# Kernel tuning notes

Measured on AMD Instinct MI355X. Metric: run time of the kernel, lower is better.

Reference implementation:

```python
import jax, jax.numpy as jnp
import numpy as np

B, C, H, W, K = 64, 64, 32, 32, 1024  # C == dim_dict, K == size_dict
BETA = 0.25


def setup_inputs() -> dict:
    key = jax.random.key(0)
    k1, k2, k3 = jax.random.split(key, 3)
    return {
        "z_from_encoder": jax.random.normal(k1, (B, C, H, W), dtype=jnp.float32),
        "codebook": jax.random.normal(k2, (K, C), dtype=jnp.float32),
        "codebook_weight": jax.random.normal(k3, (K,), dtype=jnp.float32),
        "flg_train": 1,
    }


def reference(z_from_encoder, codebook, codebook_weight, flg_train):
    # NCHW -> NHWC, flatten to (N, D)
    z = jnp.transpose(z_from_encoder, (0, 2, 3, 1))
    zf = z.reshape(-1, z.shape[-1])                      # (N, D)
    # squared euclidean distances via expansion (N, K)
    d = (jnp.sum(zf ** 2, axis=1, keepdims=True)
         + jnp.sum(codebook ** 2, axis=1)
         - 2.0 * zf @ codebook.T)
    idx = jnp.argmin(d, axis=1)                          # (N,)
    # one-hot @ codebook == gather
    z_q = codebook[idx].reshape(z.shape)                 # (B, H, W, D)
    if flg_train:
        loss = (BETA * jnp.mean((jax.lax.stop_gradient(z_q) - z) ** 2)
                + jnp.mean((z_q - jax.lax.stop_gradient(z)) ** 2))
    else:
        loss = jnp.float32(0.0)
    # straight-through estimator
    z_q_st = z + jax.lax.stop_gradient(z_q - z)
    # codebook usage histogram -> perplexity
    n_tok = zf.shape[0]
    e_mean = jnp.zeros((codebook.shape[0],), z.dtype).at[idx].add(1.0) / n_tok
    perplexity = jnp.exp(-jnp.sum(e_mean * jnp.log(e_mean + 1e-10)))
    z_q_out = jnp.transpose(z_q_st, (0, 3, 1, 2))        # back to NCHW
    return z_q_out, loss, perplexity
```

## Files before the change

### kernel.cpp

```cpp
#include <hip/hip_runtime.h>


typedef __attribute__((ext_vector_type(8))) short short8;
typedef __attribute__((ext_vector_type(4))) float float4v;

#define NELEM 4194304

#define WS_CBF   0
#define WS_C2H   262144
#define WS_HIST  266240
#define WS_LOSS  270336

__device__ __forceinline__ unsigned bf16_rne(float x) {
    unsigned u = __float_as_uint(x);
    return (u + 0x7fffu + ((u >> 16) & 1u)) >> 16;
}

__global__ __launch_bounds__(256) void prep_kernel(
    const float* __restrict__ cb, ushort* __restrict__ cbf,
    float* __restrict__ c2h, int* __restrict__ hist, float* __restrict__ loss_part) {
    __shared__ float s_c2[2][16];
    int tid  = threadIdx.x;
    int lane = tid & 63, wave = tid >> 6;
    int quad = lane >> 4, col = lane & 15;
    int bx   = blockIdx.x;

    if (bx >= 64) {
        hist[(bx - 64) * 256 + tid] = 0;
        if (bx == 64 && tid < 64) loss_part[tid] = 0.f;
        return;
    }
    int c = bx, fid = wave;
    int st = fid & 1, split = fid >> 1;
    int code  = c * 16 + col;
    int dbase = st * 32 + quad * 8;
    const float* cp = cb + code * 64 + dbase;
    float4v v0 = *(const float4v*)cp;
    float4v v1 = *(const float4v*)(cp + 4);
    float xs[8] = {v0.x, v0.y, v0.z, v0.w, v1.x, v1.y, v1.z, v1.w};
    short8 frag;
    float ssq = 0.f;
#pragma unroll
    for (int j = 0; j < 8; j++) {
        float x = xs[j];
        ssq = fmaf(x, x, ssq);
        unsigned hb = bf16_rne(x);
        if (split == 0) frag[j] = (short)hb;
        else            frag[j] = (short)bf16_rne(x - __uint_as_float(hb << 16));
    }
    *(short8*)(cbf + ((c * 4 + fid) * 64 + lane) * 8) = frag;
    if (split == 0) {
        ssq += __shfl_xor(ssq, 16);
        ssq += __shfl_xor(ssq, 32);
        if (quad == 0) s_c2[st][col] = ssq;
    }
    __syncthreads();
    if (tid < 16) c2h[c * 16 + tid] = -0.5f * (s_c2[0][tid] + s_c2[1][tid]);
}

__global__ __launch_bounds__(256, 4) void vq_kernel(
    const float* __restrict__ z, const float* __restrict__ cb,
    const ushort* __restrict__ cbf, const float* __restrict__ c2h,
    float* __restrict__ out, float* __restrict__ loss_part, int* __restrict__ hist)
{
    __shared__ float s_q[64 * 65];
    __shared__ float s_ms[2][64];
    __shared__ int   s_mi[2][64];
    __shared__ int   s_idx[64];
    __shared__ float s_red[4];

    int tid  = threadIdx.x;
    int lane = tid & 63, wave = tid >> 6;
    int quad = lane >> 4, col = lane & 15;
    int bx   = blockIdx.x;

    int tokbase = bx * 64;
    int bb = tokbase >> 10, hwb = tokbase & 1023;
    const float* zb = z + bb * 65536 + hwb;
    int tokhalf = wave & 1, khalf = wave >> 1;

    short8 ah[2][2], al[2][2];
#pragma unroll
    for (int g = 0; g < 2; g++) {
        int rel = tokhalf * 32 + g * 16 + col;
#pragma unroll
        for (int st = 0; st < 2; st++) {
            short8 h8, l8;
#pragma unroll
            for (int j = 0; j < 8; j++) {
                int d = st * 32 + quad * 8 + j;
                float x = zb[d * 1024 + rel];
                unsigned hb = bf16_rne(x);
                h8[j] = (short)hb;
                l8[j] = (short)bf16_rne(x - __uint_as_float(hb << 16));
            }
            ah[g][st] = h8; al[g][st] = l8;
        }
    }

    float best[2][4]; int bidx[2][4];
#pragma unroll
    for (int g = 0; g < 2; g++)
#pragma unroll
        for (int r = 0; r < 4; r++) { best[g][r] = -1e38f; bidx[g][r] = 0; }

    int cbase = khalf * 32;
    const ushort* cw = cbf + lane * 8;
    {
        const ushort* p0 = cw + cbase * 2048;
        short8 nb0 = *(const short8*)(p0 + 0);
        short8 nb1 = *(const short8*)(p0 + 512);
        short8 nb2 = *(const short8*)(p0 + 1024);
        short8 nb3 = *(const short8*)(p0 + 1536);
        float  nini = c2h[cbase * 16 + col];
        for (int cc = 0; cc < 32; cc++) {
            short8 bh0 = nb0, bh1 = nb1, bl0 = nb2, bl1 = nb3;
            float  ini = nini;
            if (cc < 31) {
                const ushort* np = cw + (cbase + cc + 1) * 2048;
                nb0 = *(const short8*)(np + 0);
                nb1 = *(const short8*)(np + 512);
                nb2 = *(const short8*)(np + 1024);
                nb3 = *(const short8*)(np + 1536);
                nini = c2h[(cbase + cc + 1) * 16 + col];
            }
            int code = (cbase + cc) * 16 + col;
#pragma unroll
            for (int g = 0; g < 2; g++) {
                float4v a0 = {ini, ini, ini, ini};
                float4v a1 = {0.f, 0.f, 0.f, 0.f};
                a0 = __builtin_amdgcn_mfma_f32_16x16x32_bf16(ah[g][0], bh0, a0, 0, 0, 0);
                a1 = __builtin_amdgcn_mfma_f32_16x16x32_bf16(ah[g][1], bh1, a1, 0, 0, 0);
                a0 = __builtin_amdgcn_mfma_f32_16x16x32_bf16(ah[g][0], bl0, a0, 0, 0, 0);
                a1 = __builtin_amdgcn_mfma_f32_16x16x32_bf16(ah[g][1], bl1, a1, 0, 0, 0);
                a0 = __builtin_amdgcn_mfma_f32_16x16x32_bf16(al[g][0], bh0, a0, 0, 0, 0);
                a1 = __builtin_amdgcn_mfma_f32_16x16x32_bf16(al[g][1], bh1, a1, 0, 0, 0);
                a0 = __builtin_amdgcn_mfma_f32_16x16x32_bf16(al[g][0], bl0, a0, 0, 0, 0);
                a1 = __builtin_amdgcn_mfma_f32_16x16x32_bf16(al[g][1], bl1, a1, 0, 0, 0);
#pragma unroll
                for (int r = 0; r < 4; r++) {
                    float s = a0[r] + a1[r];
                    if (s > best[g][r]) { best[g][r] = s; bidx[g][r] = code; }
                }
            }
        }
    }

#pragma unroll
    for (int g = 0; g < 2; g++) {
#pragma unroll
        for (int r = 0; r < 4; r++) {
            float s = best[g][r]; int ix = bidx[g][r];
#pragma unroll
            for (int m = 1; m <= 8; m <<= 1) {
                float so = __shfl_xor(s, m);
                int   io = __shfl_xor(ix, m);
                if (so > s || (so == s && io < ix)) { s = so; ix = io; }
            }
            if (col == 0) {
                int t = tokhalf * 32 + g * 16 + quad * 4 + r;
                s_ms[khalf][t] = s; s_mi[khalf][t] = ix;
            }
        }
    }
    __syncthreads();

    if (tid < 64) {
        float s0 = s_ms[0][tid], s1 = s_ms[1][tid];
        int   i0 = s_mi[0][tid], i1 = s_mi[1][tid];
        int   ix = (s1 > s0) ? i1 : i0;
        s_idx[tid] = ix;
        atomicAdd(&hist[ix], 1);
    }
    __syncthreads();

#pragma unroll
    for (int p = 0; p < 16; p++) {
        int i = p * 256 + tid;
        int t = i >> 6, d = i & 63;
        s_q[t * 65 + d] = cb[s_idx[t] * 64 + d];
    }
    __syncthreads();

    float ls = 0.f;
#pragma unroll 4
    for (int p = 0; p < 16; p++) {
        int i = p * 256 + tid;
        int d = i >> 6, t = i & 63;
        int a = d * 1024 + t;
        float zv = zb[a];
        float q  = s_q[t * 65 + d];
        float df = q - zv;
        out[bb * 65536 + hwb + a] = zv + df;
        ls = fmaf(df, df, ls);
    }
#pragma unroll
    for (int off = 32; off; off >>= 1) ls += __shfl_down(ls, off);
    if (lane == 0) s_red[wave] = ls;
    __syncthreads();
    if (tid == 0) {
        float v = (s_red[0] + s_red[1]) + (s_red[2] + s_red[3]);
        atomicAdd(&loss_part[bx & 63], v);
    }
}

__global__ __launch_bounds__(1024) void finalize_kernel(
    const int* __restrict__ hist, const float* __restrict__ loss_part,
    const int* __restrict__ flg, float* __restrict__ out) {
    __shared__ float red[16];
    int   k = threadIdx.x;
    float e = (float)hist[k] * (1.0f / 65536.0f);
    float v = e * logf(e + 1e-10f);
#pragma unroll
    for (int off = 32; off; off >>= 1) v += __shfl_down(v, off);
    if ((k & 63) == 0) red[k >> 6] = v;
    __syncthreads();
    if (k == 0) {
        float s = 0.f;
#pragma unroll
        for (int i = 0; i < 16; i++) s += red[i];
        out[NELEM + 1] = expf(-s);

        float ls = 0.f;
        for (int i = 0; i < 64; i++) ls += loss_part[i];
        float m    = ls * (1.0f / (float)NELEM);
        out[NELEM] = (*flg) ? (0.25f * m + m) : 0.0f;
    }
}

extern "C" void kernel_launch(void* const* d_in, const int* in_sizes, int n_in,
                              void* d_out, int out_size, void* d_ws, size_t ws_size,
                              hipStream_t stream) {
    const float* z   = (const float*)d_in[0];
    const float* cb  = (const float*)d_in[1];
    const int*   flg = (const int*)d_in[3];

    float* out = (float*)d_out;
    char*  ws  = (char*)d_ws;

    ushort* cbf       = (ushort*)(ws + WS_CBF);
    float*  c2h       = (float*)(ws + WS_C2H);
    int*    hist      = (int*)(ws + WS_HIST);
    float*  loss_part = (float*)(ws + WS_LOSS);

    prep_kernel<<<68, 256, 0, stream>>>(cb, cbf, c2h, hist, loss_part);
    vq_kernel<<<1024, 256, 0, stream>>>(z, cb, cbf, c2h, out, loss_part, hist);
    finalize_kernel<<<1, 1024, 0, stream>>>(hist, loss_part, flg, out);
}
```

Baseline: 121.2 us.

## Double tokens per block and fold finalize into last-block reduction

Each vq block now handles 128 tokens instead of 64, so every codebook fragment loaded from global memory feeds twice as many MFMAs. The grid drops to 512 blocks and the launch bound drops to 2 waves per SIMD to make room for the larger register and LDS footprint. The separate finalize kernel is removed: a global done-counter lets the last block compute perplexity and loss, saving one kernel launch. In exchange occupancy falls, there are fewer blocks than before to spread over the CUs, and the tail now includes a serial reduction in one block.

```diff
diff --git a/kernel.cpp b/kernel.cpp
--- a/kernel.cpp
+++ b/kernel.cpp
@@ -5,11 +5,13 @@
 typedef __attribute__((ext_vector_type(4))) float float4v;
 
 #define NELEM 4194304
+#define NBLK  512
 
 #define WS_CBF   0
 #define WS_C2H   262144
 #define WS_HIST  266240
 #define WS_LOSS  270336
+#define WS_DONE  270464
 
 __device__ __forceinline__ unsigned bf16_rne(float x) {
     unsigned u = __float_as_uint(x);
@@ -18,7 +20,8 @@
 
 __global__ __launch_bounds__(256) void prep_kernel(
     const float* __restrict__ cb, ushort* __restrict__ cbf,
-    float* __restrict__ c2h, int* __restrict__ hist, float* __restrict__ loss_part) {
+    float* __restrict__ c2h, int* __restrict__ hist, float* __restrict__ loss_part,
+    int* __restrict__ done) {
     __shared__ float s_c2[2][16];
     int tid  = threadIdx.x;
     int lane = tid & 63, wave = tid >> 6;
@@ -27,7 +30,10 @@
 
     if (bx >= 64) {
         hist[(bx - 64) * 256 + tid] = 0;
-        if (bx == 64 && tid < 64) loss_part[tid] = 0.f;
+        if (bx == 64) {
+            if (tid < 32)  loss_part[tid] = 0.f;
+            if (tid == 32) *done = 0;
+        }
         return;
     }
     int c = bx, fid = wave;
@@ -58,31 +64,33 @@
     if (tid < 16) c2h[c * 16 + tid] = -0.5f * (s_c2[0][tid] + s_c2[1][tid]);
 }
 
-__global__ __launch_bounds__(256, 4) void vq_kernel(
+__global__ __launch_bounds__(256, 2) void vq_kernel(
     const float* __restrict__ z, const float* __restrict__ cb,
     const ushort* __restrict__ cbf, const float* __restrict__ c2h,
-    float* __restrict__ out, float* __restrict__ loss_part, int* __restrict__ hist)
+    float* __restrict__ out, float* __restrict__ loss_part, int* __restrict__ hist,
+    int* __restrict__ done, const int* __restrict__ flg)
 {
-    __shared__ float s_q[64 * 65];
-    __shared__ float s_ms[2][64];
-    __shared__ int   s_mi[2][64];
-    __shared__ int   s_idx[64];
+    __shared__ float s_q[128 * 65];
+    __shared__ float s_ms[2][128];
+    __shared__ int   s_mi[2][128];
+    __shared__ int   s_idx[128];
     __shared__ float s_red[4];
+    __shared__ int   s_last;
 
     int tid  = threadIdx.x;
     int lane = tid & 63, wave = tid >> 6;
     int quad = lane >> 4, col = lane & 15;
     int bx   = blockIdx.x;
 
-    int tokbase = bx * 64;
+    int tokbase = bx * 128;
     int bb = tokbase >> 10, hwb = tokbase & 1023;
     const float* zb = z + bb * 65536 + hwb;
-    int tokhalf = wave & 1, khalf = wave >> 1;
-
-    short8 ah[2][2], al[2][2];
-#pragma unroll
-    for (int g = 0; g < 2; g++) {
-        int rel = tokhalf * 32 + g * 16 + col;
+    int tokgrp = wave & 1, khalf = wave >> 1;
+
+    short8 ah[4][2], al[4][2];
+#pragma unroll
+    for (int g = 0; g < 4; g++) {
+        int rel = tokgrp * 64 + g * 16 + col;
 #pragma unroll
         for (int st = 0; st < 2; st++) {
             short8 h8, l8;
@@ -98,9 +106,9 @@
         }
     }
 
-    float best[2][4]; int bidx[2][4];
-#pragma unroll
-    for (int g = 0; g < 2; g++)
+    float best[4][4]; int bidx[4][4];
+#pragma unroll
+    for (int g = 0; g < 4; g++)
 #pragma unroll
         for (int r = 0; r < 4; r++) { best[g][r] = -1e38f; bidx[g][r] = 0; }
 
@@ -126,7 +134,7 @@
             }
             int code = (cbase + cc) * 16 + col;
 #pragma unroll
-            for (int g = 0; g < 2; g++) {
+            for (int g = 0; g < 4; g++) {
                 float4v a0 = {ini, ini, ini, ini};
                 float4v a1 = {0.f, 0.f, 0.f, 0.f};
                 a0 = __builtin_amdgcn_mfma_f32_16x16x32_bf16(ah[g][0], bh0, a0, 0, 0, 0);
@@ -147,7 +155,7 @@
     }
 
 #pragma unroll
-    for (int g = 0; g < 2; g++) {
+    for (int g = 0; g < 4; g++) {
 #pragma unroll
         for (int r = 0; r < 4; r++) {
             float s = best[g][r]; int ix = bidx[g][r];
@@ -158,14 +166,14 @@
                 if (so > s || (so == s && io < ix)) { s = so; ix = io; }
             }
             if (col == 0) {
-                int t = tokhalf * 32 + g * 16 + quad * 4 + r;
+                int t = tokgrp * 64 + g * 16 + quad * 4 + r;
                 s_ms[khalf][t] = s; s_mi[khalf][t] = ix;
             }
         }
     }
     __syncthreads();
 
-    if (tid < 64) {
+    if (tid < 128) {
         float s0 = s_ms[0][tid], s1 = s_ms[1][tid];
         int   i0 = s_mi[0][tid], i1 = s_mi[1][tid];
         int   ix = (s1 > s0) ? i1 : i0;
@@ -174,8 +182,8 @@
     }
     __syncthreads();
 
-#pragma unroll
-    for (int p = 0; p < 16; p++) {
+#pragma unroll 8
+    for (int p = 0; p < 32; p++) {
         int i = p * 256 + tid;
         int t = i >> 6, d = i & 63;
         s_q[t * 65 + d] = cb[s_idx[t] * 64 + d];
@@ -184,9 +192,9 @@
 
     float ls = 0.f;
 #pragma unroll 4
-    for (int p = 0; p < 16; p++) {
+    for (int p = 0; p < 32; p++) {
         int i = p * 256 + tid;
-        int d = i >> 6, t = i & 63;
+        int d = i >> 7, t = i & 127;
         int a = d * 1024 + t;
         float zv = zb[a];
         float q  = s_q[t * 65 + d];
@@ -200,31 +208,37 @@
     __syncthreads();
     if (tid == 0) {
         float v = (s_red[0] + s_red[1]) + (s_red[2] + s_red[3]);
-        atomicAdd(&loss_part[bx & 63], v);
-    }
-}
-
-__global__ __launch_bounds__(1024) void finalize_kernel(
-    const int* __restrict__ hist, const float* __restrict__ loss_part,
-    const int* __restrict__ flg, float* __restrict__ out) {
-    __shared__ float red[16];
-    int   k = threadIdx.x;
-    float e = (float)hist[k] * (1.0f / 65536.0f);
-    float v = e * logf(e + 1e-10f);
-#pragma unroll
-    for (int off = 32; off; off >>= 1) v += __shfl_down(v, off);
-    if ((k & 63) == 0) red[k >> 6] = v;
-    __syncthreads();
-    if (k == 0) {
-        float s = 0.f;
-#pragma unroll
-        for (int i = 0; i < 16; i++) s += red[i];
-        out[NELEM + 1] = expf(-s);
-
-        float ls = 0.f;
-        for (int i = 0; i < 64; i++) ls += loss_part[i];
-        float m    = ls * (1.0f / (float)NELEM);
-        out[NELEM] = (*flg) ? (0.25f * m + m) : 0.0f;
+        atomicAdd(&loss_part[bx & 31], v);
+        __threadfence();
+        int old = __hip_atomic_fetch_add(done, 1, __ATOMIC_ACQ_REL, __HIP_MEMORY_SCOPE_AGENT);
+        s_last = (old == NBLK - 1) ? 1 : 0;
+    }
+    __syncthreads();
+
+    if (s_last) {
+        float v = 0.f;
+#pragma unroll
+        for (int rr = 0; rr < 4; rr++) {
+            int k = rr * 256 + tid;
+            float e = (float)__hip_atomic_load(&hist[k], __ATOMIC_RELAXED,
+                                               __HIP_MEMORY_SCOPE_AGENT) * (1.0f / 65536.0f);
+            v += e * logf(e + 1e-10f);
+        }
+#pragma unroll
+        for (int off = 32; off; off >>= 1) v += __shfl_down(v, off);
+        if (lane == 0) s_red[wave] = v;
+        float lsum = 0.f;
+        if (tid < 32) lsum = __hip_atomic_load(&loss_part[tid], __ATOMIC_RELAXED,
+                                               __HIP_MEMORY_SCOPE_AGENT);
+#pragma unroll
+        for (int off = 16; off; off >>= 1) lsum += __shfl_down(lsum, off);
+        __syncthreads();
+        if (tid == 0) {
+            float sE = (s_red[0] + s_red[1]) + (s_red[2] + s_red[3]);
+            out[NELEM + 1] = expf(-sE);
+            float m = lsum * (1.0f / (float)NELEM);
+            out[NELEM] = (*flg) ? (0.25f * m + m) : 0.0f;
+        }
     }
 }
 
@@ -242,8 +256,8 @@
     float*  c2h       = (float*)(ws + WS_C2H);
     int*    hist      = (int*)(ws + WS_HIST);
     float*  loss_part = (float*)(ws + WS_LOSS);
-
-    prep_kernel<<<68, 256, 0, stream>>>(cb, cbf, c2h, hist, loss_part);
-    vq_kernel<<<1024, 256, 0, stream>>>(z, cb, cbf, c2h, out, loss_part, hist);
-    finalize_kernel<<<1, 1024, 0, stream>>>(hist, loss_part, flg, out);
-}
+    int*    done      = (int*)(ws + WS_DONE);
+
+    prep_kernel<<<68, 256, 0, stream>>>(cb, cbf, c2h, hist, loss_part, done);
+    vq_kernel<<<NBLK, 256, 0, stream>>>(z, cb, cbf, c2h, out, loss_part, hist, done, flg);
+}
```

Result: slower. 153.2 us (+26.4%).
